# Kernel tuning notes

Measured on AMD Instinct MI355X. Metric: run time of the kernel, lower is better.

The kernel has to match this reference:

```python
import jax, jax.numpy as jnp
import numpy as np

EPS = 1e-5


def ternarize(w):
    # TWN: delta = 0.7*mean|w|; alpha = mean of |w| over entries above delta
    delta = 0.7 * jnp.mean(jnp.abs(w))
    mask = (jnp.abs(w) > delta).astype(w.dtype)
    alpha = jnp.sum(jnp.abs(w) * mask) / jnp.maximum(jnp.sum(mask), 1.0)
    q = alpha * jnp.sign(w) * mask
    # straight-through estimator (matches torch `w + (q - w).detach()`)
    return w + jax.lax.stop_gradient(q - w)


def conv2d(x, w, stride, pad):
    # x: NCHW, w: OIHW
    return jax.lax.conv_general_dilated(
        x, w, window_strides=(stride, stride), padding=[(pad, pad), (pad, pad)],
        dimension_numbers=("NCHW", "OIHW", "NCHW"))


def batchnorm(x, gamma, beta, mean, var):
    # inference-mode BN over channel dim of NCHW
    inv = gamma / jnp.sqrt(var + EPS)
    return x * inv[None, :, None, None] + (beta - mean * inv)[None, :, None, None]


def setup_inputs() -> dict:
    key = jax.random.key(0)
    ks = jax.random.split(key, 12)
    d = {
        "x": jax.random.normal(ks[0], (64, 3, 224, 224), jnp.float32),
        "w1": jax.random.normal(ks[1], (32, 3, 3, 3), jnp.float32) * 0.1,
        "g1": jnp.ones((32,), jnp.float32), "b1": jnp.zeros((32,), jnp.float32),
        "m1": jax.random.normal(ks[2], (32,), jnp.float32) * 0.1,
        "v1": jax.random.uniform(ks[3], (32,), jnp.float32, 0.5, 1.5),
        "w2": jax.random.normal(ks[4], (64, 32, 3, 3), jnp.float32) * 0.05,
        "g2": jnp.ones((64,), jnp.float32), "b2": jnp.zeros((64,), jnp.float32),
        "m2": jax.random.normal(ks[5], (64,), jnp.float32) * 0.1,
        "v2": jax.random.uniform(ks[6], (64,), jnp.float32, 0.5, 1.5),
        "w3": jax.random.normal(ks[7], (128, 64, 3, 3), jnp.float32) * 0.05,
        "g3": jnp.ones((128,), jnp.float32), "b3": jnp.zeros((128,), jnp.float32),
        "m3": jax.random.normal(ks[8], (128,), jnp.float32) * 0.1,
        "v3": jax.random.uniform(ks[9], (128,), jnp.float32, 0.5, 1.5),
        "wl": jax.random.normal(ks[10], (10, 128), jnp.float32) * 0.1,
        "bl": jax.random.normal(ks[11], (10,), jnp.float32) * 0.01,
    }
    return d


def reference(x, w1, g1, b1, m1, v1, w2, g2, b2, m2, v2,
              w3, g3, b3, m3, v3, wl, bl):
    h = jax.nn.relu(batchnorm(conv2d(x, ternarize(w1), 2, 1), g1, b1, m1, v1))
    h = jax.nn.relu(batchnorm(conv2d(h, ternarize(w2), 1, 1), g2, b2, m2, v2))
    h = jax.nn.relu(batchnorm(conv2d(h, ternarize(w3), 2, 1), g3, b3, m3, v3))
    h = jnp.mean(h, axis=(2, 3))  # AdaptiveAvgPool2d((1,1)) + flatten -> [N,128]
    return h @ ternarize(wl).T + bl
```

## Files before the change

kernel.cpp:

```cpp
#include <hip/hip_runtime.h>
#include <cstddef>

typedef __attribute__((ext_vector_type(8))) short short8;
typedef __attribute__((ext_vector_type(4))) float floatx4;

__device__ __forceinline__ unsigned short f2bf(float f) {
  union { float f; unsigned u; } v; v.f = f;
  const unsigned r = v.u + 0x7fffu + ((v.u >> 16) & 1u);
  return (unsigned short)(r >> 16);
}

__device__ __forceinline__ float block_reduce_sum(float v, float* sm) {
#pragma unroll
  for (int off = 32; off > 0; off >>= 1) v += __shfl_down(v, off, 64);
  const int lane = threadIdx.x & 63, wid = threadIdx.x >> 6;
  __syncthreads();
  if (lane == 0) sm[wid] = v;
  __syncthreads();
  if (threadIdx.x == 0) {
    float t = 0.f;
    const int nw = (blockDim.x + 63) >> 6;
    for (int i = 0; i < nw; ++i) t += sm[i];
    sm[0] = t;
  }
  __syncthreads();
  return sm[0];
}

__device__ __forceinline__ void tsel(int t, const float* w0, const float* w1,
                                     const float* w2, const float* w3, int n0,
                                     int n1, int n2, int n3,
                                     const float*& w, int& n) {
  w = (t == 0) ? w0 : (t == 1) ? w1 : (t == 2) ? w2 : w3;
  n = (t == 0) ? n0 : (t == 1) ? n1 : (t == 2) ? n2 : n3;
}

__global__ __launch_bounds__(256) void tern_phase1(
    const float* w0, const float* w1, const float* w2, const float* w3,
    int n0, int n1, int n2, int n3, float* __restrict__ red) {
  __shared__ float sm[8];
  const float* w; int n;
  tsel(blockIdx.y, w0, w1, w2, w3, n0, n1, n2, n3, w, n);
  if ((int)blockIdx.x * 256 >= n) return;
  const int i = blockIdx.x * 256 + threadIdx.x;
  float s = (i < n) ? fabsf(w[i]) : 0.f;
  s = block_reduce_sum(s, sm);
  if (threadIdx.x == 0) atomicAdd(&red[blockIdx.y * 4 + 0], s);
}

__global__ __launch_bounds__(256) void tern_phase2(
    const float* w0, const float* w1, const float* w2, const float* w3,
    int n0, int n1, int n2, int n3, float* __restrict__ red,
    unsigned short* __restrict__ bp1, unsigned short* __restrict__ bp2,
    unsigned short* __restrict__ bp3, float* __restrict__ ql) {
  __shared__ float sm[8];
  const float* w; int n;
  const int by = blockIdx.y;
  tsel(by, w0, w1, w2, w3, n0, n1, n2, n3, w, n);
  if ((int)blockIdx.x * 256 >= n) return;
  const float delta = 0.7f * red[by * 4 + 0] / (float)n;
  const int i = blockIdx.x * 256 + threadIdx.x;
  float c = 0.f, a = 0.f;
  float wv = 0.f;
  if (i < n) {
    wv = w[i];
    const float av = fabsf(wv);
    if (av > delta) { c = 1.f; a = av; }
  }
  if (i < n) {
    const float sgnf = (wv > delta) ? 1.f : (wv < -delta ? -1.f : 0.f);
    const unsigned short sgnb =
        (wv > delta) ? 0x3F80u : (wv < -delta ? 0xBF80u : 0u);
    if (by == 0) {
      const int k = i % 27, oc = i / 27;
      bp1[((size_t)(k >> 3) * 32 + oc) * 8 + (k & 7)] = sgnb;
    } else if (by == 1) {
      const int k = (i % 9) * 32 + (i % 288) / 9;
      bp2[((size_t)(k >> 3) * 64 + i / 288) * 8 + (k & 7)] = sgnb;
    } else if (by == 2) {
      const int k = (i % 9) * 64 + (i % 576) / 9;
      bp3[((size_t)(k >> 3) * 128 + i / 576) * 8 + (k & 7)] = sgnb;
    } else {
      ql[i] = sgnf;
    }
  }
  c = block_reduce_sum(c, sm);
  a = block_reduce_sum(a, sm);
  if (threadIdx.x == 0) {
    atomicAdd(&red[by * 4 + 1], c);
    atomicAdd(&red[by * 4 + 2], a);
  }
}

__global__ __launch_bounds__(256) void conv1_mfma(
    const float* __restrict__ x, const unsigned short* __restrict__ bp1,
    const float* __restrict__ g1, const float* __restrict__ b1,
    const float* __restrict__ m1, const float* __restrict__ v1,
    const float* __restrict__ red, unsigned short* __restrict__ y) {
  __shared__ float xs[3 * 17 * 33];
  __shared__ unsigned short im[128 * 40];
  const int n = blockIdx.y;
  const int oh0 = (blockIdx.x / 7) * 8, ow0 = (blockIdx.x % 7) * 16;
  const int t = threadIdx.x;
  const int wave = t >> 6, lane = t & 63, quad = lane >> 4, l16 = lane & 15;

  const int ihb = oh0 * 2 - 1, iwb = ow0 * 2 - 1;
  for (int i = t; i < 1683; i += 256) {
    const int ic = i / 561, r2 = i % 561;
    const int pr = r2 / 33, pc = r2 % 33;
    const int ih = ihb + pr, iw = iwb + pc;
    float v = 0.f;
    if ((unsigned)ih < 224u && (unsigned)iw < 224u)
      v = x[((size_t)n * 3 + ic) * 50176 + (size_t)ih * 224 + iw];
    xs[i] = v;
  }
  __syncthreads();

#pragma unroll
  for (int cc = 0; cc < 2; ++cc) {
    const int c = cc * 256 + t;
    const int px = c >> 2, seg = c & 3;
    const int ohl = px >> 4, owl = px & 15;
    unsigned u[4];
#pragma unroll
    for (int jj = 0; jj < 4; ++jj) {
      unsigned short lo = 0, hi = 0;
      const int k0 = seg * 8 + 2 * jj, k1 = k0 + 1;
      if (k0 < 27) {
        const int ic = k0 / 9, tp = k0 % 9;
        lo = f2bf(xs[(ic * 17 + ohl * 2 + tp / 3) * 33 + owl * 2 + tp % 3]);
      }
      if (k1 < 27) {
        const int ic = k1 / 9, tp = k1 % 9;
        hi = f2bf(xs[(ic * 17 + ohl * 2 + tp / 3) * 33 + owl * 2 + tp % 3]);
      }
      u[jj] = (unsigned)lo | ((unsigned)hi << 16);
    }
    *(uint4*)(&im[px * 40 + seg * 8]) = make_uint4(u[0], u[1], u[2], u[3]);
  }

  short8 bfr[2];
#pragma unroll
  for (int nf = 0; nf < 2; ++nf)
    bfr[nf] = *(const short8*)(bp1 + ((size_t)quad * 32 + nf * 16 + l16) * 8);

  floatx4 acc[2][2];
#pragma unroll
  for (int mi = 0; mi < 2; ++mi) {
    acc[mi][0] = (floatx4){0.f, 0.f, 0.f, 0.f};
    acc[mi][1] = (floatx4){0.f, 0.f, 0.f, 0.f};
  }
  __syncthreads();

#pragma unroll
  for (int mi = 0; mi < 2; ++mi) {
    const int pxb = (wave * 2 + mi) * 16;
    const short8 a = *(const short8*)(&im[(pxb + l16) * 40 + quad * 8]);
#pragma unroll
    for (int nf = 0; nf < 2; ++nf)
      acc[mi][nf] = __builtin_amdgcn_mfma_f32_16x16x32_bf16(
          a, bfr[nf], acc[mi][nf], 0, 0, 0);
  }

  const float alpha1 = red[2] / fmaxf(red[1], 1.f);
  float sc[2], bs[2];
#pragma unroll
  for (int nf = 0; nf < 2; ++nf) {
    const int ch = nf * 16 + l16;
    const float inv = g1[ch] / sqrtf(v1[ch] + 1e-5f);
    sc[nf] = alpha1 * inv;
    bs[nf] = b1[ch] - m1[ch] * inv;
  }
  __syncthreads();
#pragma unroll
  for (int mi = 0; mi < 2; ++mi) {
    const int ohl = wave * 2 + mi;
#pragma unroll
    for (int r = 0; r < 4; ++r) {
      const int px = ohl * 16 + quad * 4 + r;
#pragma unroll
      for (int nf = 0; nf < 2; ++nf) {
        const float vv = fmaxf(acc[mi][nf][r] * sc[nf] + bs[nf], 0.f);
        im[px * 40 + ((nf * 16 + l16) ^ (quad * 8))] = f2bf(vv);
      }
    }
  }
  __syncthreads();
#pragma unroll
  for (int i = 0; i < 2; ++i) {
    const int c = i * 256 + t;
    const int px = c >> 2, cg = c & 3;
    const int ohl = px >> 4, owl = px & 15;
    const uint4 v =
        *(const uint4*)(&im[px * 40 + ((cg ^ ((px >> 2) & 3)) * 8)]);
    *(uint4*)(y + (((size_t)n * 112 + oh0 + ohl) * 112 + ow0 + owl) * 32 +
              cg * 8) = v;
  }
}

__global__ __launch_bounds__(256, 2) void conv23_fused(
    const unsigned short* __restrict__ act1,
    const unsigned short* __restrict__ bp2,
    const unsigned short* __restrict__ bp3,
    const float* __restrict__ g2, const float* __restrict__ b2,
    const float* __restrict__ m2, const float* __restrict__ v2,
    const float* __restrict__ g3, const float* __restrict__ b3,
    const float* __restrict__ m3, const float* __restrict__ v3,
    const float* __restrict__ red, float* __restrict__ pooled) {
  __shared__ unsigned short shbuf[8 * 17 * 18 * 8];
  __shared__ float pbuf[128];
  unsigned short* a1p = shbuf;
  unsigned short* c2o = shbuf;
  const int t = threadIdx.x;
  const int img = blockIdx.y;
  const int ty = blockIdx.x / 7, tx = blockIdx.x % 7;
  const int wave = t >> 6, lane = t & 63, quad = lane >> 4, l16 = lane & 15;
  const int h0 = ty * 16 - 1, w0 = tx * 16 - 1;

  for (int c = t; c < 19 * 19 * 4; c += 256) {
    const int seg = c & 3, pix = c >> 2;
    const int ri = pix / 19, rj = pix % 19;
    const int ih = h0 - 1 + ri, iw = w0 - 1 + rj;
    uint4 v = make_uint4(0u, 0u, 0u, 0u);
    if ((unsigned)ih < 112u && (unsigned)iw < 112u)
      v = *(const uint4*)(act1 + (((size_t)img * 112 + ih) * 112 + iw) * 32 +
                          seg * 8);
    *(uint4*)(&a1p[((seg * 19 + ri) * 19 + rj) * 8]) = v;
  }

  int abase[5];
#pragma unroll
  for (int s = 0; s < 5; ++s) {
    const int mt = wave + s * 4;
    int apx = mt * 16 + l16;
    if (apx > 288) apx = 288;
    const int pi = apx / 17, pj = apx % 17;
    abase[s] = ((quad * 19 + pi) * 19 + pj) * 8;
  }
  floatx4 acc2[5][4];
#pragma unroll
  for (int s = 0; s < 5; ++s)
#pragma unroll
    for (int nf = 0; nf < 4; ++nf) acc2[s][nf] = (floatx4){0.f, 0.f, 0.f, 0.f};

  short8 bcur[4], bnxt[4];
#pragma unroll
  for (int nf = 0; nf < 4; ++nf)
    bcur[nf] = *(const short8*)(bp2 + ((size_t)quad * 64 + nf * 16 + l16) * 8);
  __syncthreads();

#pragma unroll
  for (int tap = 0; tap < 9; ++tap) {
    const int kh = tap / 3, kw = tap % 3;
    if (tap + 1 < 9) {
      const int kg = (tap + 1) * 4 + quad;
#pragma unroll
      for (int nf = 0; nf < 4; ++nf)
        bnxt[nf] =
            *(const short8*)(bp2 + ((size_t)kg * 64 + nf * 16 + l16) * 8);
    }
    const int toff = (kh * 19 + kw) * 8;
#pragma unroll
    for (int s = 0; s < 5; ++s) {
      const short8 a = *(const short8*)(&a1p[abase[s] + toff]);
#pragma unroll
      for (int nf = 0; nf < 4; ++nf)
        acc2[s][nf] = __builtin_amdgcn_mfma_f32_16x16x32_bf16(
            a, bcur[nf], acc2[s][nf], 0, 0, 0);
    }
#pragma unroll
    for (int nf = 0; nf < 4; ++nf) bcur[nf] = bnxt[nf];
  }
  __syncthreads();

  const float alpha2 = red[6] / fmaxf(red[5], 1.f);
  float sc[4], bs[4];
#pragma unroll
  for (int nf = 0; nf < 4; ++nf) {
    const int ch = nf * 16 + l16;
    const float inv = g2[ch] / sqrtf(v2[ch] + 1e-5f);
    sc[nf] = alpha2 * inv;
    bs[nf] = b2[ch] - m2[ch] * inv;
  }
  const int lo8 = l16 & 7, hs0 = l16 >> 3;
#pragma unroll
  for (int s = 0; s < 5; ++s) {
    const int mt = wave + s * 4;
#pragma unroll
    for (int r = 0; r < 4; ++r) {
      const int px = mt * 16 + quad * 4 + r;
      if (px <= 288) {
        const int pi = px / 17, pj = px % 17;
        const int slot = (pj >> 1) + (pj & 1) * 9;
        const bool inb =
            ((unsigned)(h0 + pi) < 112u) && ((unsigned)(w0 + pj) < 112u);
#pragma unroll
        for (int nf = 0; nf < 4; ++nf) {
          const float vv =
              inb ? fmaxf(acc2[s][nf][r] * sc[nf] + bs[nf], 0.f) : 0.f;
          c2o[(((nf * 2 + hs0) * 17 + pi) * 18 + slot) * 8 + lo8] = f2bf(vv);
        }
      }
    }
  }
  __syncthreads();

  int a3off[4];
#pragma unroll
  for (int mf = 0; mf < 4; ++mf) {
    const int px = mf * 16 + l16;
    a3off[mf] = ((quad * 17 + (px >> 3) * 2) * 18 + (px & 7)) * 8;
  }
  floatx4 acc3[4][2];
#pragma unroll
  for (int mf = 0; mf < 4; ++mf) {
    acc3[mf][0] = (floatx4){0.f, 0.f, 0.f, 0.f};
    acc3[mf][1] = (floatx4){0.f, 0.f, 0.f, 0.f};
  }
  short8 b3c0, b3c1, b3n0, b3n1;
  {
    const int kg = quad;
    b3c0 = *(const short8*)(bp3 + ((size_t)kg * 128 + wave * 32 + l16) * 8);
    b3c1 =
        *(const short8*)(bp3 + ((size_t)kg * 128 + wave * 32 + 16 + l16) * 8);
  }
#pragma unroll
  for (int u = 0; u < 18; ++u) {
    const int H = u / 9, tap = u % 9;
    const int kh = tap / 3, kw = tap % 3;
    if (u + 1 < 18) {
      const int H2 = (u + 1) / 9, tap2 = (u + 1) % 9;
      const int kg = tap2 * 8 + H2 * 4 + quad;
      b3n0 = *(const short8*)(bp3 + ((size_t)kg * 128 + wave * 32 + l16) * 8);
      b3n1 = *(const short8*)(bp3 +
                              ((size_t)kg * 128 + wave * 32 + 16 + l16) * 8);
    }
    const int toff = (kh * 18 + (kw >> 1) + (kw & 1) * 9) * 8 + H * 9792;
#pragma unroll
    for (int mf = 0; mf < 4; ++mf) {
      const short8 a = *(const short8*)(&c2o[a3off[mf] + toff]);
      acc3[mf][0] = __builtin_amdgcn_mfma_f32_16x16x32_bf16(
          a, b3c0, acc3[mf][0], 0, 0, 0);
      acc3[mf][1] = __builtin_amdgcn_mfma_f32_16x16x32_bf16(
          a, b3c1, acc3[mf][1], 0, 0, 0);
    }
    b3c0 = b3n0; b3c1 = b3n1;
  }

  const float alpha3 = red[10] / fmaxf(red[9], 1.f);
#pragma unroll
  for (int nf = 0; nf < 2; ++nf) {
    const int ch = wave * 32 + nf * 16 + l16;
    const float inv = g3[ch] / sqrtf(v3[ch] + 1e-5f);
    const float scv = alpha3 * inv, bsv = b3[ch] - m3[ch] * inv;
    float s = 0.f;
#pragma unroll
    for (int mf = 0; mf < 4; ++mf)
#pragma unroll
      for (int rr = 0; rr < 4; ++rr)
        s += fmaxf(acc3[mf][nf][rr] * scv + bsv, 0.f);
    s += __shfl_xor(s, 16);
    s += __shfl_xor(s, 32);
    if (lane < 16) pbuf[ch] = s;
  }
  __syncthreads();
  if (t < 128) atomicAdd(&pooled[(size_t)img * 128 + t], pbuf[t]);
}

__global__ void linear_kernel(const float* __restrict__ pooled,
                              const float* __restrict__ ql,
                              const float* __restrict__ bl,
                              const float* __restrict__ red,
                              float* __restrict__ out) {
  const int idx = blockIdx.x * blockDim.x + threadIdx.x;
  if (idx >= 64 * 10) return;
  const int n = idx / 10, o = idx % 10;
  const float* p = pooled + (size_t)n * 128;
  const float* w = ql + (size_t)o * 128;
  float s = 0.f;
#pragma unroll 4
  for (int c = 0; c < 128; ++c) s += p[c] * w[c];
  const float alpha_l = red[14] / fmaxf(red[13], 1.f);
  out[idx] = s * (alpha_l / 3136.f) + bl[o];
}

extern "C" void kernel_launch(void* const* d_in, const int* in_sizes, int n_in,
                              void* d_out, int out_size, void* d_ws,
                              size_t ws_size, hipStream_t stream) {
  const float* x  = (const float*)d_in[0];
  const float* w1 = (const float*)d_in[1];
  const float* g1 = (const float*)d_in[2];
  const float* b1 = (const float*)d_in[3];
  const float* m1 = (const float*)d_in[4];
  const float* v1 = (const float*)d_in[5];
  const float* w2 = (const float*)d_in[6];
  const float* g2 = (const float*)d_in[7];
  const float* b2 = (const float*)d_in[8];
  const float* m2 = (const float*)d_in[9];
  const float* v2 = (const float*)d_in[10];
  const float* w3 = (const float*)d_in[11];
  const float* g3 = (const float*)d_in[12];
  const float* b3 = (const float*)d_in[13];
  const float* m3 = (const float*)d_in[14];
  const float* v3 = (const float*)d_in[15];
  const float* wl = (const float*)d_in[16];
  const float* bl = (const float*)d_in[17];
  float* out = (float*)d_out;

  float* Wf = (float*)d_ws;
  float* red = Wf;
  float* pooled = red + 16;
  float* bp1f = pooled + 8192;
  float* ql = bp1f + 512;
  unsigned short* bp1 = (unsigned short*)bp1f;
  unsigned short* Us = (unsigned short*)(ql + 1280);
  unsigned short* bp2 = Us;
  unsigned short* bp3 = bp2 + 18432;
  unsigned short* act1 = bp3 + 73728;

  hipMemsetAsync(red, 0, (16 + 8192 + 512) * sizeof(float), stream);
  tern_phase1<<<dim3(288, 4), 256, 0, stream>>>(w1, w2, w3, wl, 864, 18432,
                                                73728, 1280, red);
  tern_phase2<<<dim3(288, 4), 256, 0, stream>>>(w1, w2, w3, wl, 864, 18432,
                                                73728, 1280, red, bp1, bp2,
                                                bp3, ql);

  conv1_mfma<<<dim3(98, 64), 256, 0, stream>>>(x, bp1, g1, b1, m1, v1, red,
                                               act1);
  conv23_fused<<<dim3(49, 64), 256, 0, stream>>>(act1, bp2, bp3, g2, b2, m2,
                                                 v2, g3, b3, m3, v3, red,
                                                 pooled);
  linear_kernel<<<3, 256, 0, stream>>>(pooled, ql, bl, red, out);
}
```

Measured before the change: 243.0 us.

## Double conv23_fused block to 512 threads and split work across eight waves

The fused conv2/conv3 kernel now runs with 512 threads (8 waves) per block instead of 256. Conv2 M-tiles are spread over 8 waves (3 per wave instead of 5) and conv3 output channels are split 16 per wave instead of 32. This cuts per-thread accumulators and should raise occupancy and latency hiding. In exchange each wave reloads the same A fragments from LDS for fewer MFMAs, so LDS traffic per MFMA rises, and launch bounds of 512x4 may force register spills.

```diff
diff --git a/kernel.cpp b/kernel.cpp
--- a/kernel.cpp
+++ b/kernel.cpp
@@ -198,7 +198,7 @@
   }
 }
 
-__global__ __launch_bounds__(256, 2) void conv23_fused(
+__global__ __launch_bounds__(512, 4) void conv23_fused(
     const unsigned short* __restrict__ act1,
     const unsigned short* __restrict__ bp2,
     const unsigned short* __restrict__ bp3,
@@ -217,7 +217,7 @@
   const int wave = t >> 6, lane = t & 63, quad = lane >> 4, l16 = lane & 15;
   const int h0 = ty * 16 - 1, w0 = tx * 16 - 1;
 
-  for (int c = t; c < 19 * 19 * 4; c += 256) {
+  for (int c = t; c < 19 * 19 * 4; c += 512) {
     const int seg = c & 3, pix = c >> 2;
     const int ri = pix / 19, rj = pix % 19;
     const int ih = h0 - 1 + ri, iw = w0 - 1 + rj;
@@ -228,18 +228,18 @@
     *(uint4*)(&a1p[((seg * 19 + ri) * 19 + rj) * 8]) = v;
   }
 
-  int abase[5];
-#pragma unroll
-  for (int s = 0; s < 5; ++s) {
-    const int mt = wave + s * 4;
+  int abase[3];
+#pragma unroll
+  for (int s = 0; s < 3; ++s) {
+    const int mt = wave + s * 8;
     int apx = mt * 16 + l16;
     if (apx > 288) apx = 288;
     const int pi = apx / 17, pj = apx % 17;
     abase[s] = ((quad * 19 + pi) * 19 + pj) * 8;
   }
-  floatx4 acc2[5][4];
-#pragma unroll
-  for (int s = 0; s < 5; ++s)
+  floatx4 acc2[3][4];
+#pragma unroll
+  for (int s = 0; s < 3; ++s)
 #pragma unroll
     for (int nf = 0; nf < 4; ++nf) acc2[s][nf] = (floatx4){0.f, 0.f, 0.f, 0.f};
 
@@ -261,7 +261,7 @@
     }
     const int toff = (kh * 19 + kw) * 8;
 #pragma unroll
-    for (int s = 0; s < 5; ++s) {
+    for (int s = 0; s < 3; ++s) {
       const short8 a = *(const short8*)(&a1p[abase[s] + toff]);
 #pragma unroll
       for (int nf = 0; nf < 4; ++nf)
@@ -284,8 +284,8 @@
   }
   const int lo8 = l16 & 7, hs0 = l16 >> 3;
 #pragma unroll
-  for (int s = 0; s < 5; ++s) {
-    const int mt = wave + s * 4;
+  for (int s = 0; s < 3; ++s) {
+    const int mt = wave + s * 8;
 #pragma unroll
     for (int r = 0; r < 4; ++r) {
       const int px = mt * 16 + quad * 4 + r;
@@ -311,19 +311,11 @@
     const int px = mf * 16 + l16;
     a3off[mf] = ((quad * 17 + (px >> 3) * 2) * 18 + (px & 7)) * 8;
   }
-  floatx4 acc3[4][2];
-#pragma unroll
-  for (int mf = 0; mf < 4; ++mf) {
-    acc3[mf][0] = (floatx4){0.f, 0.f, 0.f, 0.f};
-    acc3[mf][1] = (floatx4){0.f, 0.f, 0.f, 0.f};
-  }
-  short8 b3c0, b3c1, b3n0, b3n1;
-  {
-    const int kg = quad;
-    b3c0 = *(const short8*)(bp3 + ((size_t)kg * 128 + wave * 32 + l16) * 8);
-    b3c1 =
-        *(const short8*)(bp3 + ((size_t)kg * 128 + wave * 32 + 16 + l16) * 8);
-  }
+  floatx4 acc3[4];
+#pragma unroll
+  for (int mf = 0; mf < 4; ++mf) acc3[mf] = (floatx4){0.f, 0.f, 0.f, 0.f};
+  short8 b3c, b3n;
+  b3c = *(const short8*)(bp3 + ((size_t)quad * 128 + wave * 16 + l16) * 8);
 #pragma unroll
   for (int u = 0; u < 18; ++u) {
     const int H = u / 9, tap = u % 9;
@@ -331,26 +323,21 @@
     if (u + 1 < 18) {
       const int H2 = (u + 1) / 9, tap2 = (u + 1) % 9;
       const int kg = tap2 * 8 + H2 * 4 + quad;
-      b3n0 = *(const short8*)(bp3 + ((size_t)kg * 128 + wave * 32 + l16) * 8);
-      b3n1 = *(const short8*)(bp3 +
-                              ((size_t)kg * 128 + wave * 32 + 16 + l16) * 8);
+      b3n = *(const short8*)(bp3 + ((size_t)kg * 128 + wave * 16 + l16) * 8);
     }
     const int toff = (kh * 18 + (kw >> 1) + (kw & 1) * 9) * 8 + H * 9792;
 #pragma unroll
     for (int mf = 0; mf < 4; ++mf) {
       const short8 a = *(const short8*)(&c2o[a3off[mf] + toff]);
-      acc3[mf][0] = __builtin_amdgcn_mfma_f32_16x16x32_bf16(
-          a, b3c0, acc3[mf][0], 0, 0, 0);
-      acc3[mf][1] = __builtin_amdgcn_mfma_f32_16x16x32_bf16(
-          a, b3c1, acc3[mf][1], 0, 0, 0);
-    }
-    b3c0 = b3n0; b3c1 = b3n1;
+      acc3[mf] = __builtin_amdgcn_mfma_f32_16x16x32_bf16(
+          a, b3c, acc3[mf], 0, 0, 0);
+    }
+    b3c = b3n;
   }
 
   const float alpha3 = red[10] / fmaxf(red[9], 1.f);
-#pragma unroll
-  for (int nf = 0; nf < 2; ++nf) {
-    const int ch = wave * 32 + nf * 16 + l16;
+  {
+    const int ch = wave * 16 + l16;
     const float inv = g3[ch] / sqrtf(v3[ch] + 1e-5f);
     const float scv = alpha3 * inv, bsv = b3[ch] - m3[ch] * inv;
     float s = 0.f;
@@ -358,7 +345,7 @@
     for (int mf = 0; mf < 4; ++mf)
 #pragma unroll
       for (int rr = 0; rr < 4; ++rr)
-        s += fmaxf(acc3[mf][nf][rr] * scv + bsv, 0.f);
+        s += fmaxf(acc3[mf][rr] * scv + bsv, 0.f);
     s += __shfl_xor(s, 16);
     s += __shfl_xor(s, 32);
     if (lane < 16) pbuf[ch] = s;
@@ -427,7 +414,7 @@
 
   conv1_mfma<<<dim3(98, 64), 256, 0, stream>>>(x, bp1, g1, b1, m1, v1, red,
                                                act1);
-  conv23_fused<<<dim3(49, 64), 256, 0, stream>>>(act1, bp2, bp3, g2, b2, m2,
+  conv23_fused<<<dim3(49, 64), 512, 0, stream>>>(act1, bp2, bp3, g2, b2, m2,
                                                  v2, g3, b3, m3, v3, red,
                                                  pooled);
   linear_kernel<<<3, 256, 0, stream>>>(pooled, ql, bl, red, out);
```

After: 251.4 us. 1.03x slower.
